# Optimization experiments

Hardware: AMD Instinct MI355X
Metric: run time of the kernel (lower is better)

The kernel has to match this reference:

```python
import jax, jax.numpy as jnp
import numpy as np

N, E = 10000, 160000
F_IN, H1, C1, C2 = 256, 8, 128, 128
SLOPE = 0.2  # PyG GATConv default negative_slope


def setup_inputs() -> dict:
    key = jax.random.key(0)
    ks = jax.random.split(key, 9)
    s = 0.05
    return {
        "x": jax.random.normal(ks[0], (N, F_IN), jnp.float32),
        "edge_index": jax.random.randint(ks[1], (2, E), 0, N),
        "W1": jax.random.normal(ks[2], (F_IN, H1 * C1), jnp.float32) * s,
        "a_src1": jax.random.normal(ks[3], (H1, C1), jnp.float32) * s,
        "a_dst1": jax.random.normal(ks[4], (H1, C1), jnp.float32) * s,
        "b1": jnp.zeros((H1 * C1,), jnp.float32),
        "W2": jax.random.normal(ks[5], (H1 * C1, C2), jnp.float32) * s,
        "a_src2": jax.random.normal(ks[6], (1, C2), jnp.float32) * s,
        "a_dst2": jax.random.normal(ks[7], (1, C2), jnp.float32) * s,
        "b2": jnp.zeros((C2,), jnp.float32),
    }


def gat_conv(x, src, dst, W, a_s, a_d, b, heads, out_ch, concat):
    n = x.shape[0]
    h = (x @ W).reshape(n, heads, out_ch)            # [N,H,C]
    s_src = jnp.einsum("nhc,hc->nh", h, a_s)         # [N,H]
    s_dst = jnp.einsum("nhc,hc->nh", h, a_d)
    e = jax.nn.leaky_relu(s_src[src] + s_dst[dst], SLOPE)   # [Etot,H]
    # segment softmax over incoming edges per destination (self-loops guarantee non-empty segments)
    m = jax.lax.stop_gradient(jax.ops.segment_max(e, dst, num_segments=n))
    p = jnp.exp(e - m[dst])
    denom = jax.ops.segment_sum(p, dst, num_segments=n)
    alpha = p / denom[dst]                            # [Etot,H]
    out = jax.ops.segment_sum(h[src] * alpha[:, :, None], dst, num_segments=n)  # [N,H,C]
    out = out.reshape(n, heads * out_ch) if concat else out.mean(axis=1)
    return out + b


def reference(x, edge_index, W1, a_src1, a_dst1, b1, W2, a_src2, a_dst2, b2):
    n = x.shape[0]
    loops = jnp.arange(n, dtype=edge_index.dtype)     # PyG add_self_loops=True
    src = jnp.concatenate([edge_index[0], loops])
    dst = jnp.concatenate([edge_index[1], loops])
    # dropout layers are identity at inference (training=False)
    h1 = jax.nn.elu(gat_conv(x, src, dst, W1, a_src1, a_dst1, b1, H1, C1, True))
    return gat_conv(h1, src, dst, W2, a_src2, a_dst2, b2, 1, C2, False)
```

## Files before the change

### kernel.cpp

```cpp
#include <hip/hip_runtime.h>
#include <math.h>

#define F_IN 256
#define H1 8
#define C1 128
#define HC1 1024
#define C2 128
#define SLOPE 0.2f

typedef unsigned short u16;
typedef __attribute__((ext_vector_type(8))) short bf16x8;
typedef __attribute__((ext_vector_type(4))) float f32x4;
typedef __attribute__((ext_vector_type(2))) float f32x2;


__device__ __forceinline__ float lrelu(float v) { return v > 0.f ? v : SLOPE * v; }

__device__ __forceinline__ unsigned bf16_rne(float x) {
    unsigned u = __float_as_uint(x);
    u += 0x7fffu + ((u >> 16) & 1u);
    return u >> 16;
}

__device__ __forceinline__ void split2(float a, float b, unsigned& hi, unsigned& lo) {
    unsigned ha = bf16_rne(a), hb = bf16_rne(b);
    float fa = __uint_as_float(ha << 16), fb = __uint_as_float(hb << 16);
    hi = ha | (hb << 16);
    lo = bf16_rne(a - fa) | (bf16_rne(b - fb) << 16);
}

__device__ __forceinline__ void gload16(const u16* g, u16* l) {
    __builtin_amdgcn_global_load_lds(
        (const __attribute__((address_space(1))) unsigned*)g,
        (__attribute__((address_space(3))) unsigned*)l, 16, 0, 0);
}


__global__ void init_deg(int* deg, int n) {
    int i = blockIdx.x * blockDim.x + threadIdx.x;
    if (i < n) deg[i] = 1;
}

__global__ void hist_kernel(const int* __restrict__ dst, int* __restrict__ deg, int E) {
    int i = blockIdx.x * blockDim.x + threadIdx.x;
    if (i < E) atomicAdd(&deg[dst[i]], 1);
}

__global__ void scan_kernel(const int* __restrict__ deg, int* __restrict__ start,
                            int* __restrict__ cursor, int n) {
    __shared__ int buf[1024];
    int carry = 0;
    for (int base = 0; base < n; base += 1024) {
        int i = base + (int)threadIdx.x;
        int v = (i < n) ? deg[i] : 0;
        buf[threadIdx.x] = v;
        __syncthreads();
        for (int offd = 1; offd < 1024; offd <<= 1) {
            int tv = 0;
            if ((int)threadIdx.x >= offd) tv = buf[threadIdx.x - offd];
            __syncthreads();
            if ((int)threadIdx.x >= offd) buf[threadIdx.x] += tv;
            __syncthreads();
        }
        int incl = buf[threadIdx.x];
        if (i < n) { start[i] = carry + incl - v; cursor[i] = carry + incl - v; }
        carry += buf[1023];
        __syncthreads();
    }
    if (threadIdx.x == 0) start[n] = carry;
}

__global__ void scatter_kernel(const int* __restrict__ src, const int* __restrict__ dst,
                               int* __restrict__ cursor, int* __restrict__ ssorted,
                               int* __restrict__ dsorted, int E, int N) {
    int i = blockIdx.x * blockDim.x + threadIdx.x;
    if (i < E) {
        int d = dst[i];
        int pos = atomicAdd(&cursor[d], 1);
        ssorted[pos] = src[i];
        dsorted[pos] = d;
    } else if (i < E + N) {
        int d = i - E;
        int pos = atomicAdd(&cursor[d], 1);
        ssorted[pos] = d;
        dsorted[pos] = d;
    }
}


__global__ void split_mat(const float* __restrict__ in, u16* __restrict__ hi,
                          u16* __restrict__ lo, int n) {
    int i = blockIdx.x * blockDim.x + threadIdx.x;
    if (i >= n) return;
    float v = in[i];
    unsigned h = bf16_rne(v);
    hi[i] = (u16)h;
    lo[i] = (u16)bf16_rne(v - __uint_as_float(h << 16));
}

__global__ void split_transpose(const float* __restrict__ in, u16* __restrict__ hi,
                                u16* __restrict__ lo, int R, int C) {
    int i = blockIdx.x * blockDim.x + threadIdx.x;
    if (i >= R * C) return;
    int r = i / C, c = i % C;
    float v = in[i];
    unsigned h = bf16_rne(v);
    hi[(size_t)c * R + r] = (u16)h;
    lo[(size_t)c * R + r] = (u16)bf16_rne(v - __uint_as_float(h << 16));
}


__global__ __launch_bounds__(256) void gemm_mfma(const u16* __restrict__ Ahi,
                                                 const u16* __restrict__ Alo,
                                                 const u16* __restrict__ Bhi,
                                                 const u16* __restrict__ Blo,
                                                 u16* __restrict__ Cbf,
                                                 int M, int N, int K) {
    __shared__ u16 lds[16384];
    const int t = threadIdx.x;
    const int rbase = blockIdx.y * 128;
    const int cbase = blockIdx.x * 128;

    const int lane = t & 63;
    const int R0 = (t >> 7) << 6;
    const int C0 = ((t >> 6) & 1) << 6;
    const int lrow = lane & 15;
    const int kq = lane >> 4;

    f32x4 acc[4][4] = {};

    for (int k0 = 0; k0 < K; k0 += 32) {
#pragma unroll
        for (int i = 0; i < 2; i++) {
            int c = t + (i << 8);
            int row = c >> 2;
            int kc = (c & 3) << 3;
            int ar = min(rbase + row, M - 1);
            int br = cbase + row;
            gload16(Ahi + (size_t)ar * K + k0 + kc, &lds[c * 8]);
            gload16(Alo + (size_t)ar * K + k0 + kc, &lds[4096 + c * 8]);
            gload16(Bhi + (size_t)br * K + k0 + kc, &lds[8192 + c * 8]);
            gload16(Blo + (size_t)br * K + k0 + kc, &lds[12288 + c * 8]);
        }
        __syncthreads();

        bf16x8 ah[4], al[4], bh[4], bl[4];
#pragma unroll
        for (int m = 0; m < 4; m++) {
            int off = (R0 + (m << 4) + lrow) * 32 + (kq << 3);
            ah[m] = *(const bf16x8*)&lds[off];
            al[m] = *(const bf16x8*)&lds[4096 + off];
        }
#pragma unroll
        for (int n = 0; n < 4; n++) {
            int off = (C0 + (n << 4) + lrow) * 32 + (kq << 3);
            bh[n] = *(const bf16x8*)&lds[8192 + off];
            bl[n] = *(const bf16x8*)&lds[12288 + off];
        }
#pragma unroll
        for (int m = 0; m < 4; m++)
#pragma unroll
            for (int n = 0; n < 4; n++) {
                acc[m][n] = __builtin_amdgcn_mfma_f32_16x16x32_bf16(ah[m], bh[n], acc[m][n], 0, 0, 0);
                acc[m][n] = __builtin_amdgcn_mfma_f32_16x16x32_bf16(ah[m], bl[n], acc[m][n], 0, 0, 0);
                acc[m][n] = __builtin_amdgcn_mfma_f32_16x16x32_bf16(al[m], bh[n], acc[m][n], 0, 0, 0);
            }
        __syncthreads();
    }

#pragma unroll
    for (int m = 0; m < 4; m++)
#pragma unroll
        for (int n = 0; n < 4; n++) {
            int col = cbase + C0 + (n << 4) + lrow;
#pragma unroll
            for (int r = 0; r < 4; r++) {
                int row = rbase + R0 + (m << 4) + kq * 4 + r;
                if (row < M) Cbf[(size_t)row * N + col] = (u16)bf16_rne(acc[m][n][r]);
            }
        }
}


__global__ __launch_bounds__(256) void gemm_mfma64(const u16* __restrict__ Ahi,
                                                   const u16* __restrict__ Alo,
                                                   const u16* __restrict__ Bhi,
                                                   const u16* __restrict__ Blo,
                                                   u16* __restrict__ Cbf,
                                                   int M, int N, int K) {
    __shared__ u16 lds[8192];
    const int t = threadIdx.x;
    const int rbase = blockIdx.y * 64;
    const int cbase = blockIdx.x * 64;

    const int lane = t & 63;
    const int w = t >> 6;
    const int R0 = (w >> 1) << 5;
    const int C0 = (w & 1) << 5;
    const int lrow = lane & 15;
    const int kq = lane >> 4;

    f32x4 acc[2][2] = {};

    for (int k0 = 0; k0 < K; k0 += 32) {
        {
            int row = t >> 2;
            int kc = (t & 3) << 3;
            int ar = min(rbase + row, M - 1);
            int br = cbase + row;
            gload16(Ahi + (size_t)ar * K + k0 + kc, &lds[t * 8]);
            gload16(Alo + (size_t)ar * K + k0 + kc, &lds[2048 + t * 8]);
            gload16(Bhi + (size_t)br * K + k0 + kc, &lds[4096 + t * 8]);
            gload16(Blo + (size_t)br * K + k0 + kc, &lds[6144 + t * 8]);
        }
        __syncthreads();

        bf16x8 ah[2], al[2], bh[2], bl[2];
#pragma unroll
        for (int m = 0; m < 2; m++) {
            int off = (R0 + (m << 4) + lrow) * 32 + (kq << 3);
            ah[m] = *(const bf16x8*)&lds[off];
            al[m] = *(const bf16x8*)&lds[2048 + off];
        }
#pragma unroll
        for (int n = 0; n < 2; n++) {
            int off = (C0 + (n << 4) + lrow) * 32 + (kq << 3);
            bh[n] = *(const bf16x8*)&lds[4096 + off];
            bl[n] = *(const bf16x8*)&lds[6144 + off];
        }
#pragma unroll
        for (int m = 0; m < 2; m++)
#pragma unroll
            for (int n = 0; n < 2; n++) {
                acc[m][n] = __builtin_amdgcn_mfma_f32_16x16x32_bf16(ah[m], bh[n], acc[m][n], 0, 0, 0);
                acc[m][n] = __builtin_amdgcn_mfma_f32_16x16x32_bf16(ah[m], bl[n], acc[m][n], 0, 0, 0);
                acc[m][n] = __builtin_amdgcn_mfma_f32_16x16x32_bf16(al[m], bh[n], acc[m][n], 0, 0, 0);
            }
        __syncthreads();
    }

#pragma unroll
    for (int m = 0; m < 2; m++)
#pragma unroll
        for (int n = 0; n < 2; n++) {
            int col = cbase + C0 + (n << 4) + lrow;
#pragma unroll
            for (int r = 0; r < 4; r++) {
                int row = rbase + R0 + (m << 4) + kq * 4 + r;
                if (row < M) Cbf[(size_t)row * N + col] = (u16)bf16_rne(acc[m][n][r]);
            }
        }
}


__global__ __launch_bounds__(256) void scores1_bf(const unsigned* __restrict__ hbf,
                                                  const float* __restrict__ a_s,
                                                  const float* __restrict__ a_d,
                                                  float* __restrict__ ssrc,
                                                  float* __restrict__ sdst, int N) {
    int wid = blockIdx.x * 4 + (threadIdx.x >> 6);
    if (wid >= N * H1) return;
    int lane = threadIdx.x & 63;
    int n = wid >> 3, hh = wid & 7;
    unsigned u = hbf[(size_t)n * 512 + hh * 64 + lane];
    float c0 = __uint_as_float(u << 16);
    float c1 = __uint_as_float(u & 0xffff0000u);
    const float* as = a_s + hh * C1;
    const float* ad = a_d + hh * C1;
    float vs = c0 * as[2 * lane] + c1 * as[2 * lane + 1];
    float vd = c0 * ad[2 * lane] + c1 * ad[2 * lane + 1];
    for (int off = 32; off; off >>= 1) {
        vs += __shfl_xor(vs, off);
        vd += __shfl_xor(vd, off);
    }
    if (lane == 0) { ssrc[wid] = vs; sdst[wid] = vd; }
}

__global__ __launch_bounds__(256) void scores2_bf(const unsigned* __restrict__ hbf,
                                                  const float* __restrict__ a_s,
                                                  const float* __restrict__ a_d,
                                                  float* __restrict__ ssrc,
                                                  float* __restrict__ sdst, int N) {
    int n = blockIdx.x * 4 + (threadIdx.x >> 6);
    if (n >= N) return;
    int lane = threadIdx.x & 63;
    unsigned u = hbf[(size_t)n * 64 + lane];
    float c0 = __uint_as_float(u << 16);
    float c1 = __uint_as_float(u & 0xffff0000u);
    float vs = c0 * a_s[2 * lane] + c1 * a_s[2 * lane + 1];
    float vd = c0 * a_d[2 * lane] + c1 * a_d[2 * lane + 1];
    for (int off = 32; off; off >>= 1) {
        vs += __shfl_xor(vs, off);
        vd += __shfl_xor(vd, off);
    }
    if (lane == 0) { ssrc[n] = vs; sdst[n] = vd; }
}


__global__ __launch_bounds__(256) void edgep1(const int* __restrict__ ssorted,
                                              const int* __restrict__ dsorted,
                                              const float* __restrict__ ssrc,
                                              const float* __restrict__ sdst,
                                              float* __restrict__ p, int Et) {
    int e = blockIdx.x * 256 + threadIdx.x;
    if (e >= Et) return;
    int sr = ssorted[e], dr = dsorted[e];
    float4 s0 = ((const float4*)(ssrc + sr * 8))[0];
    float4 s1 = ((const float4*)(ssrc + sr * 8))[1];
    float4 d0 = ((const float4*)(sdst + dr * 8))[0];
    float4 d1 = ((const float4*)(sdst + dr * 8))[1];
    float4 r0, r1;
    r0.x = __expf(lrelu(s0.x + d0.x));
    r0.y = __expf(lrelu(s0.y + d0.y));
    r0.z = __expf(lrelu(s0.z + d0.z));
    r0.w = __expf(lrelu(s0.w + d0.w));
    r1.x = __expf(lrelu(s1.x + d1.x));
    r1.y = __expf(lrelu(s1.y + d1.y));
    r1.z = __expf(lrelu(s1.z + d1.z));
    r1.w = __expf(lrelu(s1.w + d1.w));
    ((float4*)(p + (size_t)e * 8))[0] = r0;
    ((float4*)(p + (size_t)e * 8))[1] = r1;
}

__global__ __launch_bounds__(256) void edgep2(const int* __restrict__ ssorted,
                                              const int* __restrict__ dsorted,
                                              const float* __restrict__ ssrc,
                                              const float* __restrict__ sdst,
                                              float* __restrict__ p, int Et) {
    int e = blockIdx.x * 256 + threadIdx.x;
    if (e >= Et) return;
    p[e] = __expf(lrelu(ssrc[ssorted[e]] + sdst[dsorted[e]]));
}


__global__ __launch_bounds__(256) void denom1(const float* __restrict__ p,
                                              const int* __restrict__ start,
                                              float* __restrict__ dinv, int N) {
    int t = blockIdx.x * 256 + threadIdx.x;
    if (t >= N * 8) return;
    int d = t >> 3, h = t & 7;
    int s0 = start[d], ne = start[d + 1] - s0;
    float s = 0.f;
    for (int e = 0; e < ne; e++) s += p[(size_t)(s0 + e) * 8 + h];
    dinv[t] = 1.f / s;
}

__global__ __launch_bounds__(256) void denom2(const float* __restrict__ p,
                                              const int* __restrict__ start,
                                              float* __restrict__ dinv, int N) {
    int d = blockIdx.x * 256 + threadIdx.x;
    if (d >= N) return;
    int s0 = start[d], ne = start[d + 1] - s0;
    float s = 0.f;
    for (int e = 0; e < ne; e++) s += p[s0 + e];
    dinv[d] = 1.f / s;
}


__global__ __launch_bounds__(256) void alphaoff1(const int* __restrict__ ssorted,
                                                 const int* __restrict__ dsorted,
                                                 const float* __restrict__ p,
                                                 const float* __restrict__ dinv,
                                                 int2* __restrict__ aoff,
                                                 int Et, int Etp) {
    int e = blockIdx.x * 256 + threadIdx.x;
    if (e >= Etp) return;
    if (e >= Et) {
#pragma unroll
        for (int h = 0; h < 8; h++) aoff[(size_t)h * Etp + e] = make_int2(0, 0);
        return;
    }
    int sr = ssorted[e], dr = dsorted[e];
    int srb = sr * 2048;
    float4 p0 = ((const float4*)(p + (size_t)e * 8))[0];
    float4 p1v = ((const float4*)(p + (size_t)e * 8))[1];
    float4 i0 = ((const float4*)(dinv + (size_t)dr * 8))[0];
    float4 i1 = ((const float4*)(dinv + (size_t)dr * 8))[1];
    aoff[(size_t)0 * Etp + e] = make_int2(srb +    0, __float_as_int(p0.x * i0.x));
    aoff[(size_t)1 * Etp + e] = make_int2(srb +  256, __float_as_int(p0.y * i0.y));
    aoff[(size_t)2 * Etp + e] = make_int2(srb +  512, __float_as_int(p0.z * i0.z));
    aoff[(size_t)3 * Etp + e] = make_int2(srb +  768, __float_as_int(p0.w * i0.w));
    aoff[(size_t)4 * Etp + e] = make_int2(srb + 1024, __float_as_int(p1v.x * i1.x));
    aoff[(size_t)5 * Etp + e] = make_int2(srb + 1280, __float_as_int(p1v.y * i1.y));
    aoff[(size_t)6 * Etp + e] = make_int2(srb + 1536, __float_as_int(p1v.z * i1.z));
    aoff[(size_t)7 * Etp + e] = make_int2(srb + 1792, __float_as_int(p1v.w * i1.w));
}

__global__ __launch_bounds__(256) void alphaoff2(const int* __restrict__ ssorted,
                                                 const int* __restrict__ dsorted,
                                                 const float* __restrict__ p,
                                                 const float* __restrict__ dinv,
                                                 int2* __restrict__ aoff,
                                                 int Et, int Etp) {
    int e = blockIdx.x * 256 + threadIdx.x;
    if (e >= Etp) return;
    if (e >= Et) { aoff[e] = make_int2(0, 0); return; }
    aoff[e] = make_int2(ssorted[e] * 256, __float_as_int(p[e] * dinv[dsorted[e]]));
}


template<int H, bool SPLITOUT>
__global__ __launch_bounds__(256) void agg_gather(const char* __restrict__ hbytes,
                                                  const int2* __restrict__ aoff,
                                                  const int* __restrict__ start,
                                                  const float* __restrict__ bias,
                                                  float* __restrict__ out,
                                                  unsigned* __restrict__ outHi,
                                                  unsigned* __restrict__ outLo,
                                                  int N, int Etp) {
    int hh, grp;
    if (H == 8) { hh = blockIdx.x & 7; grp = blockIdx.x >> 3; }
    else        { hh = 0;              grp = blockIdx.x; }
    int wid = threadIdx.x >> 6, lane = threadIdx.x & 63;
    int d = grp * 4 + wid;
    if (d >= N) return;
    const int g = lane >> 4, p16 = lane & 15;
    int s0 = start[d];
    int ne = start[d + 1] - s0;
    const int2* base = aoff + (size_t)hh * Etp + s0;
    const char* hb = hbytes + p16 * 16;

    f32x2 acc0 = {0.f, 0.f}, acc1 = {0.f, 0.f}, acc2 = {0.f, 0.f}, acc3 = {0.f, 0.f};
#pragma unroll 2
    for (int e2 = 0; e2 < ne; e2 += 4) {
        int2 pr = base[e2 + g];
        float a = (e2 + g < ne) ? __int_as_float(pr.y) : 0.f;
        uint4 u = *(const uint4*)(hb + pr.x);
        f32x2 av = {a, a};
        f32x2 f0 = {__uint_as_float(u.x << 16), __uint_as_float(u.x & 0xffff0000u)};
        f32x2 f1 = {__uint_as_float(u.y << 16), __uint_as_float(u.y & 0xffff0000u)};
        f32x2 f2 = {__uint_as_float(u.z << 16), __uint_as_float(u.z & 0xffff0000u)};
        f32x2 f3 = {__uint_as_float(u.w << 16), __uint_as_float(u.w & 0xffff0000u)};
        acc0 += av * f0;
        acc1 += av * f1;
        acc2 += av * f2;
        acc3 += av * f3;
    }

    float acc[8] = {acc0.x, acc0.y, acc1.x, acc1.y, acc2.x, acc2.y, acc3.x, acc3.y};
#pragma unroll
    for (int i = 0; i < 8; i++) {
        acc[i] += __shfl_xor(acc[i], 16);
        acc[i] += __shfl_xor(acc[i], 32);
    }

    float r0 = g == 0 ? acc[0] : g == 1 ? acc[2] : g == 2 ? acc[4] : acc[6];
    float r1 = g == 0 ? acc[1] : g == 1 ? acc[3] : g == 2 ? acc[5] : acc[7];
    int j = 4 * p16 + g;
    float2 bv = ((const float2*)bias)[hh * 64 + j];
    r0 += bv.x; r1 += bv.y;
    size_t idx = (size_t)d * (H * 64) + hh * 64 + j;
    if (SPLITOUT) {
        r0 = r0 > 0.f ? r0 : expm1f(r0);
        r1 = r1 > 0.f ? r1 : expm1f(r1);
        unsigned hi, lo;
        split2(r0, r1, hi, lo);
        outHi[idx] = hi;
        outLo[idx] = lo;
    } else {
        ((float2*)out)[idx] = make_float2(r0, r1);
    }
}


extern "C" void kernel_launch(void* const* d_in, const int* in_sizes, int n_in,
                              void* d_out, int out_size, void* d_ws, size_t ws_size,
                              hipStream_t stream) {
    const float* x      = (const float*)d_in[0];
    const int*   ei     = (const int*)d_in[1];
    const float* W1     = (const float*)d_in[2];
    const float* a_src1 = (const float*)d_in[3];
    const float* a_dst1 = (const float*)d_in[4];
    const float* b1     = (const float*)d_in[5];
    const float* W2     = (const float*)d_in[6];
    const float* a_src2 = (const float*)d_in[7];
    const float* a_dst2 = (const float*)d_in[8];
    const float* b2     = (const float*)d_in[9];
    float* out = (float*)d_out;

    int E = in_sizes[1] / 2;
    int N = in_sizes[0] / F_IN;
    int Et = E + N;
    int Etp = Et + 4;
    const int* esrc = ei;
    const int* edst = ei + E;

    char* ws = (char*)d_ws;
    size_t off = 0;
    auto alloc = [&](size_t bytes) -> char* {
        char* p = ws + off;
        off = (off + bytes + 255) & ~(size_t)255;
        return p;
    };
    u16* x_hi    = (u16*)alloc((size_t)N * F_IN * 2);
    u16* x_lo    = (u16*)alloc((size_t)N * F_IN * 2);
    u16* W1t_hi  = (u16*)alloc((size_t)F_IN * HC1 * 2);
    u16* W1t_lo  = (u16*)alloc((size_t)F_IN * HC1 * 2);
    u16* W2t_hi  = (u16*)alloc((size_t)HC1 * C2 * 2);
    u16* W2t_lo  = (u16*)alloc((size_t)HC1 * C2 * 2);
    u16* h1_bf   = (u16*)alloc((size_t)N * HC1 * 2);
    u16* h1a_hi  = (u16*)alloc((size_t)N * HC1 * 2);
    u16* h1a_lo  = (u16*)alloc((size_t)N * HC1 * 2);
    u16* h2_bf   = (u16*)alloc((size_t)N * C2 * 2);
    float* ss1   = (float*)alloc((size_t)N * H1 * 4);
    float* sd1   = (float*)alloc((size_t)N * H1 * 4);
    float* ss2   = (float*)alloc((size_t)N * 4);
    float* sd2   = (float*)alloc((size_t)N * 4);
    float* p1    = (float*)alloc((size_t)Et * H1 * 4);
    float* p2    = (float*)alloc((size_t)Et * 4);
    float* dinv1 = (float*)alloc((size_t)N * H1 * 4);
    float* dinv2 = (float*)alloc((size_t)N * 4);
    int2* aoff1  = (int2*)alloc((size_t)Etp * H1 * 8);
    int2* aoff2  = (int2*)alloc((size_t)Etp * 8);
    int* deg     = (int*)alloc((size_t)N * 4);
    int* startp  = (int*)alloc((size_t)(N + 1) * 4);
    int* cursor  = (int*)alloc((size_t)N * 4);
    int* ssorted = (int*)alloc((size_t)Et * 4);
    int* dsorted = (int*)alloc((size_t)Et * 4);

    init_deg<<<(N + 255) / 256, 256, 0, stream>>>(deg, N);
    hist_kernel<<<(E + 255) / 256, 256, 0, stream>>>(edst, deg, E);
    scan_kernel<<<1, 1024, 0, stream>>>(deg, startp, cursor, N);
    scatter_kernel<<<(Et + 255) / 256, 256, 0, stream>>>(esrc, edst, cursor, ssorted, dsorted, E, N);

    split_mat<<<(N * F_IN + 255) / 256, 256, 0, stream>>>(x, x_hi, x_lo, N * F_IN);
    split_transpose<<<(F_IN * HC1 + 255) / 256, 256, 0, stream>>>(W1, W1t_hi, W1t_lo, F_IN, HC1);
    split_transpose<<<(HC1 * C2 + 255) / 256, 256, 0, stream>>>(W2, W2t_hi, W2t_lo, HC1, C2);

    gemm_mfma<<<dim3(HC1 / 128, (N + 127) / 128), 256, 0, stream>>>(
        x_hi, x_lo, W1t_hi, W1t_lo, h1_bf, N, HC1, F_IN);
    scores1_bf<<<(N * H1 + 3) / 4, 256, 0, stream>>>(
        (const unsigned*)h1_bf, a_src1, a_dst1, ss1, sd1, N);
    edgep1<<<(Et + 255) / 256, 256, 0, stream>>>(ssorted, dsorted, ss1, sd1, p1, Et);
    denom1<<<(N * H1 + 255) / 256, 256, 0, stream>>>(p1, startp, dinv1, N);
    alphaoff1<<<(Etp + 255) / 256, 256, 0, stream>>>(ssorted, dsorted, p1, dinv1, aoff1, Et, Etp);
    agg_gather<H1, true><<<((N + 3) / 4) * H1, 256, 0, stream>>>(
        (const char*)h1_bf, aoff1, startp, b1,
        nullptr, (unsigned*)h1a_hi, (unsigned*)h1a_lo, N, Etp);

    gemm_mfma64<<<dim3(C2 / 64, (N + 63) / 64), 256, 0, stream>>>(
        h1a_hi, h1a_lo, W2t_hi, W2t_lo, h2_bf, N, C2, HC1);
    scores2_bf<<<(N + 3) / 4, 256, 0, stream>>>(
        (const unsigned*)h2_bf, a_src2, a_dst2, ss2, sd2, N);
    edgep2<<<(Et + 255) / 256, 256, 0, stream>>>(ssorted, dsorted, ss2, sd2, p2, Et);
    denom2<<<(N + 255) / 256, 256, 0, stream>>>(p2, startp, dinv2, N);
    alphaoff2<<<(Etp + 255) / 256, 256, 0, stream>>>(ssorted, dsorted, p2, dinv2, aoff2, Et, Etp);
    agg_gather<1, false><<<(N + 3) / 4, 256, 0, stream>>>(
        (const char*)h2_bf, aoff2, startp, b2,
        out, nullptr, nullptr, N, Etp);
}
```

Measured before the change: 275.6 us.

## Drop lo split of layer-1 activations, fuse prep kernels, atomic denominators, faster scan

Several changes at once. The second GEMM now reads a single bf16 copy of the ELU output instead of a hi/lo split, which removes one MFMA per tile, one LDS stream and half of the activation writes and reads. The three split/transpose kernels are merged into one prep launch. The serial per-node denominator loops are replaced by atomic adds in the edge kernels followed by a reciprocal pass, and the 1024-wide blocked scan becomes a 256-thread chunked scan. Activation precision drops to plain bf16, and the atomic float sums make results order-dependent.

Result: slower. 368.9 us (+33.9%).

```diff
diff --git a/kernel.cpp b/kernel.cpp
--- a/kernel.cpp
+++ b/kernel.cpp
@@ -22,11 +22,8 @@
     return u >> 16;
 }
 
-__device__ __forceinline__ void split2(float a, float b, unsigned& hi, unsigned& lo) {
-    unsigned ha = bf16_rne(a), hb = bf16_rne(b);
-    float fa = __uint_as_float(ha << 16), fb = __uint_as_float(hb << 16);
-    hi = ha | (hb << 16);
-    lo = bf16_rne(a - fa) | (bf16_rne(b - fb) << 16);
+__device__ __forceinline__ unsigned pack2_bf16(float a, float b) {
+    return bf16_rne(a) | (bf16_rne(b) << 16);
 }
 
 __device__ __forceinline__ void gload16(const u16* g, u16* l) {
@@ -36,9 +33,10 @@
 }
 
 
-__global__ void init_deg(int* deg, int n) {
-    int i = blockIdx.x * blockDim.x + threadIdx.x;
-    if (i < n) deg[i] = 1;
+__global__ void init_kernel(int* deg, float* den1, float* den2, int N) {
+    int i = blockIdx.x * 256 + threadIdx.x;
+    if (i < N * 8) den1[i] = 0.f;
+    if (i < N) { deg[i] = 1; den2[i] = 0.f; }
 }
 
 __global__ void hist_kernel(const int* __restrict__ dst, int* __restrict__ deg, int E) {
@@ -46,28 +44,28 @@
     if (i < E) atomicAdd(&deg[dst[i]], 1);
 }
 
-__global__ void scan_kernel(const int* __restrict__ deg, int* __restrict__ start,
-                            int* __restrict__ cursor, int n) {
-    __shared__ int buf[1024];
-    int carry = 0;
-    for (int base = 0; base < n; base += 1024) {
-        int i = base + (int)threadIdx.x;
-        int v = (i < n) ? deg[i] : 0;
-        buf[threadIdx.x] = v;
+__global__ void scan_small(const int* __restrict__ deg, int* __restrict__ start,
+                           int* __restrict__ cursor, int n) {
+    __shared__ int sums[256];
+    int t = threadIdx.x;
+    int per = (n + 255) / 256;
+    int lo = t * per, hi = min(lo + per, n);
+    int s = 0;
+    for (int i = lo; i < hi; i++) s += deg[i];
+    sums[t] = s;
+    __syncthreads();
+    for (int off = 1; off < 256; off <<= 1) {
+        int v = (t >= off) ? sums[t - off] : 0;
         __syncthreads();
-        for (int offd = 1; offd < 1024; offd <<= 1) {
-            int tv = 0;
-            if ((int)threadIdx.x >= offd) tv = buf[threadIdx.x - offd];
-            __syncthreads();
-            if ((int)threadIdx.x >= offd) buf[threadIdx.x] += tv;
-            __syncthreads();
-        }
-        int incl = buf[threadIdx.x];
-        if (i < n) { start[i] = carry + incl - v; cursor[i] = carry + incl - v; }
-        carry += buf[1023];
+        sums[t] += v;
         __syncthreads();
     }
-    if (threadIdx.x == 0) start[n] = carry;
+    int run = (t == 0) ? 0 : sums[t - 1];
+    for (int i = lo; i < hi; i++) {
+        start[i] = run; cursor[i] = run;
+        run += deg[i];
+    }
+    if (t == 255) start[n] = sums[255];
 }
 
 __global__ void scatter_kernel(const int* __restrict__ src, const int* __restrict__ dst,
@@ -88,25 +86,37 @@
 }
 
 
-__global__ void split_mat(const float* __restrict__ in, u16* __restrict__ hi,
-                          u16* __restrict__ lo, int n) {
-    int i = blockIdx.x * blockDim.x + threadIdx.x;
-    if (i >= n) return;
-    float v = in[i];
-    unsigned h = bf16_rne(v);
-    hi[i] = (u16)h;
-    lo[i] = (u16)bf16_rne(v - __uint_as_float(h << 16));
-}
-
-__global__ void split_transpose(const float* __restrict__ in, u16* __restrict__ hi,
-                                u16* __restrict__ lo, int R, int C) {
-    int i = blockIdx.x * blockDim.x + threadIdx.x;
-    if (i >= R * C) return;
-    int r = i / C, c = i % C;
-    float v = in[i];
-    unsigned h = bf16_rne(v);
-    hi[(size_t)c * R + r] = (u16)h;
-    lo[(size_t)c * R + r] = (u16)bf16_rne(v - __uint_as_float(h << 16));
+__global__ void prep(const float* __restrict__ x, const float* __restrict__ W1,
+                     const float* __restrict__ W2,
+                     u16* __restrict__ x_hi, u16* __restrict__ x_lo,
+                     u16* __restrict__ W1t_hi, u16* __restrict__ W1t_lo,
+                     u16* __restrict__ W2t_hi, u16* __restrict__ W2t_lo, int N) {
+    int i = blockIdx.x * 256 + threadIdx.x;
+    int nx = N * F_IN;
+    if (i < nx) {
+        float v = x[i];
+        unsigned h = bf16_rne(v);
+        x_hi[i] = (u16)h;
+        x_lo[i] = (u16)bf16_rne(v - __uint_as_float(h << 16));
+        return;
+    }
+    i -= nx;
+    if (i < F_IN * HC1) {
+        int r = i / HC1, c = i % HC1;
+        float v = W1[i];
+        unsigned h = bf16_rne(v);
+        W1t_hi[(size_t)c * F_IN + r] = (u16)h;
+        W1t_lo[(size_t)c * F_IN + r] = (u16)bf16_rne(v - __uint_as_float(h << 16));
+        return;
+    }
+    i -= F_IN * HC1;
+    if (i < HC1 * C2) {
+        int r = i / C2, c = i % C2;
+        float v = W2[i];
+        unsigned h = bf16_rne(v);
+        W2t_hi[(size_t)c * HC1 + r] = (u16)h;
+        W2t_lo[(size_t)c * HC1 + r] = (u16)bf16_rne(v - __uint_as_float(h << 16));
+    }
 }
 
 
@@ -182,13 +192,12 @@
 }
 
 
-__global__ __launch_bounds__(256) void gemm_mfma64(const u16* __restrict__ Ahi,
-                                                   const u16* __restrict__ Alo,
-                                                   const u16* __restrict__ Bhi,
-                                                   const u16* __restrict__ Blo,
-                                                   u16* __restrict__ Cbf,
-                                                   int M, int N, int K) {
-    __shared__ u16 lds[8192];
+__global__ __launch_bounds__(256) void gemm_mfma64b(const u16* __restrict__ A,
+                                                    const u16* __restrict__ Bhi,
+                                                    const u16* __restrict__ Blo,
+                                                    u16* __restrict__ Cbf,
+                                                    int M, int N, int K) {
+    __shared__ u16 lds[6144];
     const int t = threadIdx.x;
     const int rbase = blockIdx.y * 64;
     const int cbase = blockIdx.x * 64;
@@ -208,25 +217,23 @@
             int kc = (t & 3) << 3;
             int ar = min(rbase + row, M - 1);
             int br = cbase + row;
-            gload16(Ahi + (size_t)ar * K + k0 + kc, &lds[t * 8]);
-            gload16(Alo + (size_t)ar * K + k0 + kc, &lds[2048 + t * 8]);
-            gload16(Bhi + (size_t)br * K + k0 + kc, &lds[4096 + t * 8]);
-            gload16(Blo + (size_t)br * K + k0 + kc, &lds[6144 + t * 8]);
+            gload16(A + (size_t)ar * K + k0 + kc, &lds[t * 8]);
+            gload16(Bhi + (size_t)br * K + k0 + kc, &lds[2048 + t * 8]);
+            gload16(Blo + (size_t)br * K + k0 + kc, &lds[4096 + t * 8]);
         }
         __syncthreads();
 
-        bf16x8 ah[2], al[2], bh[2], bl[2];
+        bf16x8 ah[2], bh[2], bl[2];
 #pragma unroll
         for (int m = 0; m < 2; m++) {
             int off = (R0 + (m << 4) + lrow) * 32 + (kq << 3);
             ah[m] = *(const bf16x8*)&lds[off];
-            al[m] = *(const bf16x8*)&lds[2048 + off];
         }
 #pragma unroll
         for (int n = 0; n < 2; n++) {
             int off = (C0 + (n << 4) + lrow) * 32 + (kq << 3);
-            bh[n] = *(const bf16x8*)&lds[4096 + off];
-            bl[n] = *(const bf16x8*)&lds[6144 + off];
+            bh[n] = *(const bf16x8*)&lds[2048 + off];
+            bl[n] = *(const bf16x8*)&lds[4096 + off];
         }
 #pragma unroll
         for (int m = 0; m < 2; m++)
@@ -234,7 +241,6 @@
             for (int n = 0; n < 2; n++) {
                 acc[m][n] = __builtin_amdgcn_mfma_f32_16x16x32_bf16(ah[m], bh[n], acc[m][n], 0, 0, 0);
                 acc[m][n] = __builtin_amdgcn_mfma_f32_16x16x32_bf16(ah[m], bl[n], acc[m][n], 0, 0, 0);
-                acc[m][n] = __builtin_amdgcn_mfma_f32_16x16x32_bf16(al[m], bh[n], acc[m][n], 0, 0, 0);
             }
         __syncthreads();
     }
@@ -297,11 +303,12 @@
 }
 
 
-__global__ __launch_bounds__(256) void edgep1(const int* __restrict__ ssorted,
-                                              const int* __restrict__ dsorted,
-                                              const float* __restrict__ ssrc,
-                                              const float* __restrict__ sdst,
-                                              float* __restrict__ p, int Et) {
+__global__ __launch_bounds__(256) void edgepd1(const int* __restrict__ ssorted,
+                                               const int* __restrict__ dsorted,
+                                               const float* __restrict__ ssrc,
+                                               const float* __restrict__ sdst,
+                                               float* __restrict__ p,
+                                               float* __restrict__ den, int Et) {
     int e = blockIdx.x * 256 + threadIdx.x;
     if (e >= Et) return;
     int sr = ssorted[e], dr = dsorted[e];
@@ -320,40 +327,30 @@
     r1.w = __expf(lrelu(s1.w + d1.w));
     ((float4*)(p + (size_t)e * 8))[0] = r0;
     ((float4*)(p + (size_t)e * 8))[1] = r1;
-}
-
-__global__ __launch_bounds__(256) void edgep2(const int* __restrict__ ssorted,
-                                              const int* __restrict__ dsorted,
-                                              const float* __restrict__ ssrc,
-                                              const float* __restrict__ sdst,
-                                              float* __restrict__ p, int Et) {
+    float* dn = den + dr * 8;
+    atomicAdd(dn + 0, r0.x); atomicAdd(dn + 1, r0.y);
+    atomicAdd(dn + 2, r0.z); atomicAdd(dn + 3, r0.w);
+    atomicAdd(dn + 4, r1.x); atomicAdd(dn + 5, r1.y);
+    atomicAdd(dn + 6, r1.z); atomicAdd(dn + 7, r1.w);
+}
+
+__global__ __launch_bounds__(256) void edgepd2(const int* __restrict__ ssorted,
+                                               const int* __restrict__ dsorted,
+                                               const float* __restrict__ ssrc,
+                                               const float* __restrict__ sdst,
+                                               float* __restrict__ p,
+                                               float* __restrict__ den, int Et) {
     int e = blockIdx.x * 256 + threadIdx.x;
     if (e >= Et) return;
-    p[e] = __expf(lrelu(ssrc[ssorted[e]] + sdst[dsorted[e]]));
-}
-
-
-__global__ __launch_bounds__(256) void denom1(const float* __restrict__ p,
-                                              const int* __restrict__ start,
-                                              float* __restrict__ dinv, int N) {
-    int t = blockIdx.x * 256 + threadIdx.x;
-    if (t >= N * 8) return;
-    int d = t >> 3, h = t & 7;
-    int s0 = start[d], ne = start[d + 1] - s0;
-    float s = 0.f;
-    for (int e = 0; e < ne; e++) s += p[(size_t)(s0 + e) * 8 + h];
-    dinv[t] = 1.f / s;
-}
-
-__global__ __launch_bounds__(256) void denom2(const float* __restrict__ p,
-                                              const int* __restrict__ start,
-                                              float* __restrict__ dinv, int N) {
-    int d = blockIdx.x * 256 + threadIdx.x;
-    if (d >= N) return;
-    int s0 = start[d], ne = start[d + 1] - s0;
-    float s = 0.f;
-    for (int e = 0; e < ne; e++) s += p[s0 + e];
-    dinv[d] = 1.f / s;
+    int dr = dsorted[e];
+    float v = __expf(lrelu(ssrc[ssorted[e]] + sdst[dr]));
+    p[e] = v;
+    atomicAdd(den + dr, v);
+}
+
+__global__ void rcp_kernel(float* __restrict__ v, int n) {
+    int i = blockIdx.x * 256 + threadIdx.x;
+    if (i < n) v[i] = 1.f / v[i];
 }
 
 
@@ -399,14 +396,13 @@
 }
 
 
-template<int H, bool SPLITOUT>
+template<int H, bool BF16OUT>
 __global__ __launch_bounds__(256) void agg_gather(const char* __restrict__ hbytes,
                                                   const int2* __restrict__ aoff,
                                                   const int* __restrict__ start,
                                                   const float* __restrict__ bias,
                                                   float* __restrict__ out,
-                                                  unsigned* __restrict__ outHi,
-                                                  unsigned* __restrict__ outLo,
+                                                  unsigned* __restrict__ outBf,
                                                   int N, int Etp) {
     int hh, grp;
     if (H == 8) { hh = blockIdx.x & 7; grp = blockIdx.x >> 3; }
@@ -450,13 +446,10 @@
     float2 bv = ((const float2*)bias)[hh * 64 + j];
     r0 += bv.x; r1 += bv.y;
     size_t idx = (size_t)d * (H * 64) + hh * 64 + j;
-    if (SPLITOUT) {
+    if (BF16OUT) {
         r0 = r0 > 0.f ? r0 : expm1f(r0);
         r1 = r1 > 0.f ? r1 : expm1f(r1);
-        unsigned hi, lo;
-        split2(r0, r1, hi, lo);
-        outHi[idx] = hi;
-        outLo[idx] = lo;
+        outBf[idx] = pack2_bf16(r0, r1);
     } else {
         ((float2*)out)[idx] = make_float2(r0, r1);
     }
@@ -499,8 +492,7 @@
     u16* W2t_hi  = (u16*)alloc((size_t)HC1 * C2 * 2);
     u16* W2t_lo  = (u16*)alloc((size_t)HC1 * C2 * 2);
     u16* h1_bf   = (u16*)alloc((size_t)N * HC1 * 2);
-    u16* h1a_hi  = (u16*)alloc((size_t)N * HC1 * 2);
-    u16* h1a_lo  = (u16*)alloc((size_t)N * HC1 * 2);
+    u16* h1a_bf  = (u16*)alloc((size_t)N * HC1 * 2);
     u16* h2_bf   = (u16*)alloc((size_t)N * C2 * 2);
     float* ss1   = (float*)alloc((size_t)N * H1 * 4);
     float* sd1   = (float*)alloc((size_t)N * H1 * 4);
@@ -508,8 +500,8 @@
     float* sd2   = (float*)alloc((size_t)N * 4);
     float* p1    = (float*)alloc((size_t)Et * H1 * 4);
     float* p2    = (float*)alloc((size_t)Et * 4);
-    float* dinv1 = (float*)alloc((size_t)N * H1 * 4);
-    float* dinv2 = (float*)alloc((size_t)N * 4);
+    float* den1  = (float*)alloc((size_t)N * H1 * 4);
+    float* den2  = (float*)alloc((size_t)N * 4);
     int2* aoff1  = (int2*)alloc((size_t)Etp * H1 * 8);
     int2* aoff2  = (int2*)alloc((size_t)Etp * 8);
     int* deg     = (int*)alloc((size_t)N * 4);
@@ -518,34 +510,32 @@
     int* ssorted = (int*)alloc((size_t)Et * 4);
     int* dsorted = (int*)alloc((size_t)Et * 4);
 
-    init_deg<<<(N + 255) / 256, 256, 0, stream>>>(deg, N);
+    init_kernel<<<(N * 8 + 255) / 256, 256, 0, stream>>>(deg, den1, den2, N);
     hist_kernel<<<(E + 255) / 256, 256, 0, stream>>>(edst, deg, E);
-    scan_kernel<<<1, 1024, 0, stream>>>(deg, startp, cursor, N);
+    scan_small<<<1, 256, 0, stream>>>(deg, startp, cursor, N);
     scatter_kernel<<<(Et + 255) / 256, 256, 0, stream>>>(esrc, edst, cursor, ssorted, dsorted, E, N);
 
-    split_mat<<<(N * F_IN + 255) / 256, 256, 0, stream>>>(x, x_hi, x_lo, N * F_IN);
-    split_transpose<<<(F_IN * HC1 + 255) / 256, 256, 0, stream>>>(W1, W1t_hi, W1t_lo, F_IN, HC1);
-    split_transpose<<<(HC1 * C2 + 255) / 256, 256, 0, stream>>>(W2, W2t_hi, W2t_lo, HC1, C2);
+    int prep_n = N * F_IN + F_IN * HC1 + HC1 * C2;
+    prep<<<(prep_n + 255) / 256, 256, 0, stream>>>(
+        x, W1, W2, x_hi, x_lo, W1t_hi, W1t_lo, W2t_hi, W2t_lo, N);
 
     gemm_mfma<<<dim3(HC1 / 128, (N + 127) / 128), 256, 0, stream>>>(
         x_hi, x_lo, W1t_hi, W1t_lo, h1_bf, N, HC1, F_IN);
     scores1_bf<<<(N * H1 + 3) / 4, 256, 0, stream>>>(
         (const unsigned*)h1_bf, a_src1, a_dst1, ss1, sd1, N);
-    edgep1<<<(Et + 255) / 256, 256, 0, stream>>>(ssorted, dsorted, ss1, sd1, p1, Et);
-    denom1<<<(N * H1 + 255) / 256, 256, 0, stream>>>(p1, startp, dinv1, N);
-    alphaoff1<<<(Etp + 255) / 256, 256, 0, stream>>>(ssorted, dsorted, p1, dinv1, aoff1, Et, Etp);
+    edgepd1<<<(Et + 255) / 256, 256, 0, stream>>>(ssorted, dsorted, ss1, sd1, p1, den1, Et);
+    rcp_kernel<<<(N * 8 + 255) / 256, 256, 0, stream>>>(den1, N * 8);
+    alphaoff1<<<(Etp + 255) / 256, 256, 0, stream>>>(ssorted, dsorted, p1, den1, aoff1, Et, Etp);
     agg_gather<H1, true><<<((N + 3) / 4) * H1, 256, 0, stream>>>(
-        (const char*)h1_bf, aoff1, startp, b1,
-        nullptr, (unsigned*)h1a_hi, (unsigned*)h1a_lo, N, Etp);
-
-    gemm_mfma64<<<dim3(C2 / 64, (N + 63) / 64), 256, 0, stream>>>(
-        h1a_hi, h1a_lo, W2t_hi, W2t_lo, h2_bf, N, C2, HC1);
+        (const char*)h1_bf, aoff1, startp, b1, nullptr, (unsigned*)h1a_bf, N, Etp);
+
+    gemm_mfma64b<<<dim3(C2 / 64, (N + 63) / 64), 256, 0, stream>>>(
+        h1a_bf, W2t_hi, W2t_lo, h2_bf, N, C2, HC1);
     scores2_bf<<<(N + 3) / 4, 256, 0, stream>>>(
         (const unsigned*)h2_bf, a_src2, a_dst2, ss2, sd2, N);
-    edgep2<<<(Et + 255) / 256, 256, 0, stream>>>(ssorted, dsorted, ss2, sd2, p2, Et);
-    denom2<<<(N + 255) / 256, 256, 0, stream>>>(p2, startp, dinv2, N);
-    alphaoff2<<<(Etp + 255) / 256, 256, 0, stream>>>(ssorted, dsorted, p2, dinv2, aoff2, Et, Etp);
+    edgepd2<<<(Et + 255) / 256, 256, 0, stream>>>(ssorted, dsorted, ss2, sd2, p2, den2, Et);
+    rcp_kernel<<<(N + 255) / 256, 256, 0, stream>>>(den2, N);
+    alphaoff2<<<(Etp + 255) / 256, 256, 0, stream>>>(ssorted, dsorted, p2, den2, aoff2, Et, Etp);
     agg_gather<1, false><<<(N + 3) / 4, 256, 0, stream>>>(
-        (const char*)h2_bf, aoff2, startp, b2,
-        out, nullptr, nullptr, N, Etp);
-}
+        (const char*)h2_bf, aoff2, startp, b2, out, nullptr, N, Etp);
+}
```
